# Performance work log

Measured on AMD Instinct MI355X. Metric: run time of the kernel, lower is better.

Reference implementation:

```python
import jax, jax.numpy as jnp
import numpy as np

N_NODES = 50000
N_EDGES = 800000
D_FEAT = 64
K_HOPS = 8


def setup_inputs() -> dict:
    key = jax.random.key(0)
    k1, k2 = jax.random.split(key)
    feature = jax.random.normal(k1, (N_NODES, D_FEAT), dtype=jnp.float32)
    edge_index = jax.random.randint(k2, (2, N_EDGES), 0, N_NODES, dtype=jnp.int32)
    return {"feature": feature, "edge_index": edge_index}


def reference(feature, edge_index):
    # with A_hat = D^{-1/2} (A + I) D^{-1/2} (add_remaining_self_loops + sym_norm).
    n = feature.shape[0]
    src, dst = edge_index[0], edge_index[1]
    # add_remaining_self_loops: drop any existing self-loop edges (weight -> 0)
    # and append a self loop of weight fill_value=1 for every node. Zeroing the
    # weight is mathematically identical to removing the edge.
    ew = jnp.where(src == dst, 0.0, 1.0).astype(feature.dtype)
    loop = jnp.arange(n, dtype=src.dtype)
    row = jnp.concatenate([src, loop])          # message source (x_j)
    col = jnp.concatenate([dst, loop])          # aggregation target (i)
    w = jnp.concatenate([ew, jnp.ones((n,), dtype=feature.dtype)])
    # symmetric normalization: deg over row, norm = d^-1/2[row] * w * d^-1/2[col]
    deg = jax.ops.segment_sum(w, row, num_segments=n)
    deg_inv_sqrt = jnp.where(deg > 0, jax.lax.rsqrt(deg), 0.0)
    norm = deg_inv_sqrt[row] * w * deg_inv_sqrt[col]  # [E+N]

    xs = [feature]
    x = feature
    for _ in range(K_HOPS):  # small fixed K, structural loop
        # gather-scale-scatter_add: out[i] = sum_{(j,i) in E} norm * x[j]
        x = jax.ops.segment_sum(norm[:, None] * x[row], col, num_segments=n)
        xs.append(x)
    return jnp.concatenate(xs, axis=1)  # [N, (K+1)*D]
```

## Files before the change

### kernel.cpp

```cpp
#include <hip/hip_runtime.h>
#include <hip/hip_fp16.h>

#define N_NODES 50000
#define N_EDGES 800000
#define D_FEAT 64
#define K_HOPS 8
#define OUT_STRIDE ((K_HOPS + 1) * D_FEAT)
#define NXCD 8
#define NPART 64
#define PART_CHUNK (N_EDGES / NPART)
#define NWORD (N_NODES / 2)

#define ALIGN256(x) (((x) + 255) & ~(size_t)255)
static const size_t OFF_HISTS = 0;
static const size_t OFF_AUX   = ALIGN256(OFF_HISTS + (size_t)NXCD * N_NODES * 4);
static const size_t AUX_END   = OFF_AUX + (size_t)N_EDGES * 4;
static const size_t XA_BYTES  = (size_t)(N_NODES + 1) * D_FEAT * 2;
static const size_t OFF_XA    = 0;
static const size_t OFF_DINV  = ALIGN256(AUX_END > XA_BYTES ? AUX_END : XA_BYTES);
static const size_t OFF_OFF   = ALIGN256(OFF_DINV  + (size_t)N_NODES * 4);
static const size_t OFF_BSUM  = ALIGN256(OFF_OFF   + (size_t)(N_NODES + 1) * 4);
static const size_t OFF_BASES = ALIGN256(OFF_BSUM  + 64 * 4);
static const size_t OFF_CSR   = ALIGN256(OFF_BASES + (size_t)NXCD * N_NODES * 4);
static const size_t OFF_XB    = ALIGN256(OFF_CSR   + (size_t)N_EDGES * 4);
static const size_t OFF_PART  = OFF_XB;

#define SCAN_BLOCK_ELEMS 1024
#define SCAN_NB ((N_NODES + SCAN_BLOCK_ELEMS - 1) / SCAN_BLOCK_ELEMS)

__device__ __forceinline__ unsigned xcc_id() {
    return __builtin_amdgcn_s_getreg((31u << 11) | 20u) & (NXCD - 1);
}

__device__ __forceinline__ unsigned pack_h2(float a, float b) {
    union { __half2 h; unsigned u; } c;
    c.h = __floats2half2_rn(a, b);
    return c.u;
}
__device__ __forceinline__ float2 unpack_h2(unsigned u) {
    union { unsigned u; __half2 h; } c;
    c.u = u;
    return __half22float2(c.h);
}


__global__ void k_count(const int* __restrict__ src, const int* __restrict__ dst,
                        int* __restrict__ hists, int* __restrict__ aux) {
    int e = blockIdx.x * blockDim.x + threadIdx.x;
    if (e >= N_EDGES) return;
    int s = src[e], d = dst[e];
    if (s == d) { aux[e] = -1; return; }
    unsigned x = xcc_id();
    int pw = __hip_atomic_fetch_add(&hists[x * N_NODES + d], 1,
                                    __ATOMIC_RELAXED, __HIP_MEMORY_SCOPE_WORKGROUP);
    aux[e] = (int)((x << 28) | (unsigned)pw);
}

__global__ __launch_bounds__(256, 1) void k_srcdeg(const int* __restrict__ src,
                                                   const int* __restrict__ dst,
                                                   unsigned* __restrict__ part) {
    __shared__ unsigned h[NWORD];
    int t = threadIdx.x;
    for (int w = t; w < NWORD; w += 256) h[w] = 0u;
    __syncthreads();
    int base = blockIdx.x * PART_CHUNK;
    for (int j = t; j < PART_CHUNK; j += 256) {
        int e = base + j;
        int s = src[e], d = dst[e];
        if (s != d) atomicAdd(&h[s >> 1], (s & 1) ? 65536u : 1u);
    }
    __syncthreads();
    unsigned* out = part + (size_t)blockIdx.x * NWORD;
    for (int w = t; w < NWORD; w += 256) out[w] = h[w];
}

__global__ void k_deg(const unsigned* __restrict__ part, float* __restrict__ dinv) {
    int w = blockIdx.x * blockDim.x + threadIdx.x;
    if (w >= NWORD) return;
    unsigned s0 = 0, s1 = 0, s2 = 0, s3 = 0;
    #pragma unroll 4
    for (int b = 0; b < NPART; b += 4) {
        s0 += part[(size_t)(b + 0) * NWORD + w];
        s1 += part[(size_t)(b + 1) * NWORD + w];
        s2 += part[(size_t)(b + 2) * NWORD + w];
        s3 += part[(size_t)(b + 3) * NWORD + w];
    }
    unsigned s = (s0 + s1) + (s2 + s3);
    dinv[2 * w + 0] = rsqrtf((float)((s & 0xffffu) + 1u));
    dinv[2 * w + 1] = rsqrtf((float)((s >> 16) + 1u));
}

__global__ void k_scan_sums(const int* __restrict__ hists, int* __restrict__ bsum) {
    __shared__ int lds[256];
    int b = blockIdx.x, t = threadIdx.x;
    int base = b * SCAN_BLOCK_ELEMS;
    int s = 0;
    for (int j = t; j < SCAN_BLOCK_ELEMS; j += 256) {
        int idx = base + j;
        if (idx < N_NODES) {
            #pragma unroll
            for (int c = 0; c < NXCD; ++c) s += hists[c * N_NODES + idx];
        }
    }
    lds[t] = s; __syncthreads();
    for (int str = 128; str > 0; str >>= 1) {
        if (t < str) lds[t] += lds[t + str];
        __syncthreads();
    }
    if (t == 0) bsum[b] = lds[0];
}

__global__ void k_scan_top(int* __restrict__ bsum) {
    int lane = threadIdx.x;
    int orig = (lane < SCAN_NB) ? bsum[lane] : 0;
    int v = orig;
    for (int d = 1; d < 64; d <<= 1) {
        int u = __shfl_up(v, d, 64);
        if (lane >= d) v += u;
    }
    if (lane < SCAN_NB) bsum[lane] = v - orig;
}

__global__ void k_scan_down(const int* __restrict__ hists, const int* __restrict__ bsum,
                            int* __restrict__ off, int* __restrict__ bases) {
    __shared__ int lds[256];
    int b = blockIdx.x, t = threadIdx.x;
    int base = b * SCAN_BLOCK_ELEMS + t * 4;
    int tot[4];
    #pragma unroll
    for (int j = 0; j < 4; ++j) {
        int idx = base + j; int s = 0;
        if (idx < N_NODES) {
            #pragma unroll
            for (int c = 0; c < NXCD; ++c) s += hists[c * N_NODES + idx];
        }
        tot[j] = s;
    }
    int tsum = tot[0] + tot[1] + tot[2] + tot[3];
    lds[t] = tsum; __syncthreads();
    int x = tsum;
    for (int d = 1; d < 256; d <<= 1) {
        int u = (t >= d) ? lds[t - d] : 0;
        __syncthreads();
        x += u;
        lds[t] = x;
        __syncthreads();
    }
    int p = (x - tsum) + bsum[b];
    #pragma unroll
    for (int j = 0; j < 4; ++j) {
        int idx = base + j;
        if (idx < N_NODES) {
            off[idx] = p;
            #pragma unroll
            for (int c = 0; c < NXCD; ++c) {
                bases[c * N_NODES + idx] = p;
                p += hists[c * N_NODES + idx];
            }
        } else if (idx == N_NODES) {
            off[idx] = p;
        }
    }
}

__global__ void k_scatter(const int* __restrict__ src, const int* __restrict__ dst,
                          const int* __restrict__ aux, const int* __restrict__ bases,
                          int* __restrict__ csr) {
    int e = blockIdx.x * blockDim.x + threadIdx.x;
    if (e >= N_EDGES) return;
    int a = aux[e];
    if (a < 0) return;
    int s = src[e], d = dst[e];
    unsigned x = (unsigned)a >> 28;
    int pw = a & 0x0FFFFFFF;
    int pos = bases[x * N_NODES + d] + pw;
    csr[pos] = s;
}


__global__ void k_x0(const float4* __restrict__ feat4, float4* __restrict__ out4,
                     uint2* __restrict__ y0, const float* __restrict__ dinv) {
    int t = blockIdx.x * blockDim.x + threadIdx.x;
    if (t >= (N_NODES + 1) * 16) return;
    int row = t >> 4;
    if (row < N_NODES) {
        float4 v = feat4[t];
        out4[(size_t)row * (OUT_STRIDE / 4) + (t & 15)] = v;
        float di = dinv[row];
        uint2 w;
        w.x = pack_h2(v.x * di, v.y * di);
        w.y = pack_h2(v.z * di, v.w * di);
        y0[t] = w;
    } else {
        y0[t] = make_uint2(0u, 0u);
    }
}

template <bool WRITE_HALF>
__global__ __launch_bounds__(256) void k_hop4(
    const uint2* __restrict__ yin,
    float4* __restrict__ outcol4,
    uint2* __restrict__ yout,
    const int* __restrict__ off, const int* __restrict__ csr,
    const float* __restrict__ dinv) {
    int qw = (blockIdx.x * blockDim.x + threadIdx.x) >> 6;
    int lane = threadIdx.x & 63;
    int f = lane & 15;
    int node = qw * 4 + (lane >> 4);
    int e0 = off[node], e1 = off[node + 1];
    float di = dinv[node];
    uint2 sv = yin[node * 16 + f];
    float2 lo = unpack_h2(sv.x), hi = unpack_h2(sv.y);
    float a0 = lo.x, a1 = lo.y, a2 = hi.x, a3 = hi.y;

    int nm = e1 - e0;
    #pragma unroll
    for (int d = 32; d; d >>= 1) nm = max(nm, __shfl_xor(nm, d, 64));

    auto FETCH = [&](int j) -> int {
        int idx = e0 + j;
        int c = csr[idx < e1 ? idx : 0];
        return (idx < e1) ? c : N_NODES;
    };

    int c0 = FETCH(0), c1 = FETCH(1), c2 = FETCH(2), c3 = FETCH(3);
    int c4 = FETCH(4), c5 = FETCH(5), c6 = FETCH(6), c7 = FETCH(7);
    for (int j = 0; j < nm; j += 8) {
        int d0 = FETCH(j + 8),  d1 = FETCH(j + 9),  d2 = FETCH(j + 10), d3 = FETCH(j + 11);
        int d4 = FETCH(j + 12), d5 = FETCH(j + 13), d6 = FETCH(j + 14), d7 = FETCH(j + 15);
        uint2 q0 = yin[c0 * 16 + f];
        uint2 q1 = yin[c1 * 16 + f];
        uint2 q2 = yin[c2 * 16 + f];
        uint2 q3 = yin[c3 * 16 + f];
        uint2 q4 = yin[c4 * 16 + f];
        uint2 q5 = yin[c5 * 16 + f];
        uint2 q6 = yin[c6 * 16 + f];
        uint2 q7 = yin[c7 * 16 + f];
        float2 t;
        t = unpack_h2(q0.x); a0 += t.x; a1 += t.y;
        t = unpack_h2(q0.y); a2 += t.x; a3 += t.y;
        t = unpack_h2(q1.x); a0 += t.x; a1 += t.y;
        t = unpack_h2(q1.y); a2 += t.x; a3 += t.y;
        t = unpack_h2(q2.x); a0 += t.x; a1 += t.y;
        t = unpack_h2(q2.y); a2 += t.x; a3 += t.y;
        t = unpack_h2(q3.x); a0 += t.x; a1 += t.y;
        t = unpack_h2(q3.y); a2 += t.x; a3 += t.y;
        t = unpack_h2(q4.x); a0 += t.x; a1 += t.y;
        t = unpack_h2(q4.y); a2 += t.x; a3 += t.y;
        t = unpack_h2(q5.x); a0 += t.x; a1 += t.y;
        t = unpack_h2(q5.y); a2 += t.x; a3 += t.y;
        t = unpack_h2(q6.x); a0 += t.x; a1 += t.y;
        t = unpack_h2(q6.y); a2 += t.x; a3 += t.y;
        t = unpack_h2(q7.x); a0 += t.x; a1 += t.y;
        t = unpack_h2(q7.y); a2 += t.x; a3 += t.y;
        c0 = d0; c1 = d1; c2 = d2; c3 = d3;
        c4 = d4; c5 = d5; c6 = d6; c7 = d7;
    }

    outcol4[(size_t)node * (OUT_STRIDE / 4) + f] =
        make_float4(di * a0, di * a1, di * a2, di * a3);
    if (WRITE_HALF) {
        float di2 = di * di;
        uint2 w;
        w.x = pack_h2(di2 * a0, di2 * a1);
        w.y = pack_h2(di2 * a2, di2 * a3);
        yout[node * 16 + f] = w;
        if (blockIdx.x == 0 && threadIdx.x < 16)
            yout[N_NODES * 16 + threadIdx.x] = make_uint2(0u, 0u);
    }
}


extern "C" void kernel_launch(void* const* d_in, const int* in_sizes, int n_in,
                              void* d_out, int out_size, void* d_ws, size_t ws_size,
                              hipStream_t stream) {
    const float* feature = (const float*)d_in[0];
    const int* edge = (const int*)d_in[1];
    const int* src = edge;
    const int* dst = edge + N_EDGES;
    float* out = (float*)d_out;
    char* ws = (char*)d_ws;

    int*      hists = (int*)(ws + OFF_HISTS);
    int*      aux   = (int*)(ws + OFF_AUX);
    unsigned* part  = (unsigned*)(ws + OFF_PART);
    float*    dinv  = (float*)(ws + OFF_DINV);
    int*      off   = (int*)(ws + OFF_OFF);
    int*      bsum  = (int*)(ws + OFF_BSUM);
    int*      bases = (int*)(ws + OFF_BASES);
    int*      csr   = (int*)(ws + OFF_CSR);
    uint2*    xa    = (uint2*)(ws + OFF_XA);
    uint2*    xb    = (uint2*)(ws + OFF_XB);

    const int TB = 256;
    hipMemsetAsync(ws + OFF_HISTS, 0, (size_t)NXCD * N_NODES * 4, stream);
    k_count<<<(N_EDGES + TB - 1) / TB, TB, 0, stream>>>(src, dst, hists, aux);
    k_srcdeg<<<NPART, 256, 0, stream>>>(src, dst, part);
    k_deg<<<(NWORD + TB - 1) / TB, TB, 0, stream>>>(part, dinv);
    k_x0<<<((N_NODES + 1) * 16 + TB - 1) / TB, TB, 0, stream>>>(
        (const float4*)feature, (float4*)out, xb, dinv);
    k_scan_sums<<<SCAN_NB, 256, 0, stream>>>(hists, bsum);
    k_scan_top<<<1, 64, 0, stream>>>(bsum);
    k_scan_down<<<SCAN_NB, 256, 0, stream>>>(hists, bsum, off, bases);
    k_scatter<<<(N_EDGES + TB - 1) / TB, TB, 0, stream>>>(src, dst, aux, bases, csr);
    const int hop_blocks = (N_NODES / 4) * 64 / TB;
    for (int k = 1; k <= K_HOPS; ++k) {
        const uint2* yin = (k & 1) ? xb : xa;
        uint2* yout      = (k & 1) ? xa : xb;
        float4* outcol4 = (float4*)out + (size_t)k * 16;
        if (k < K_HOPS)
            k_hop4<true><<<hop_blocks, TB, 0, stream>>>(yin, outcol4, yout, off, csr, dinv);
        else
            k_hop4<false><<<hop_blocks, TB, 0, stream>>>(yin, outcol4, nullptr, off, csr, dinv);
    }
}
```

Measured before the change: 344.1 us.

## Build CSR with per-block LDS histograms instead of global atomics

Replaces the global-atomic, XCD-partitioned destination counting and aux buffer with 128 per-block LDS histograms (packed 16-bit counts) for both source and destination degrees. The scan then derives per-block bases from those partials, and the scatter recomputes local offsets with LDS atomics. The aim is to remove contended global atomics and the memset. The cost is much larger partial arrays: k_scan_down loops over 128 partitions per node and writes 128×N bases, and the scatter only has 128 blocks. The hop kernel's gather unroll is also cut from 8 to 4.

New measurement: 400.9 us. 1.17x slower.

```diff
diff --git a/kernel.cpp b/kernel.cpp
--- a/kernel.cpp
+++ b/kernel.cpp
@@ -6,31 +6,23 @@
 #define D_FEAT 64
 #define K_HOPS 8
 #define OUT_STRIDE ((K_HOPS + 1) * D_FEAT)
-#define NXCD 8
-#define NPART 64
-#define PART_CHUNK (N_EDGES / NPART)
+#define NPART 128
+#define CHUNK (N_EDGES / NPART)
 #define NWORD (N_NODES / 2)
 
+#define SCAN_WORDS 512
+#define SCAN_NB ((NWORD + SCAN_WORDS - 1) / SCAN_WORDS)
+
 #define ALIGN256(x) (((x) + 255) & ~(size_t)255)
-static const size_t OFF_HISTS = 0;
-static const size_t OFF_AUX   = ALIGN256(OFF_HISTS + (size_t)NXCD * N_NODES * 4);
-static const size_t AUX_END   = OFF_AUX + (size_t)N_EDGES * 4;
-static const size_t XA_BYTES  = (size_t)(N_NODES + 1) * D_FEAT * 2;
-static const size_t OFF_XA    = 0;
-static const size_t OFF_DINV  = ALIGN256(AUX_END > XA_BYTES ? AUX_END : XA_BYTES);
-static const size_t OFF_OFF   = ALIGN256(OFF_DINV  + (size_t)N_NODES * 4);
+static const size_t OFF_PSRC  = 0;
+static const size_t OFF_PDST  = OFF_PSRC  + (size_t)NPART * NWORD * 4;
+static const size_t OFF_BASES = OFF_PDST  + (size_t)NPART * NWORD * 4;
+static const size_t OFF_OFF   = ALIGN256(OFF_BASES + (size_t)NPART * N_NODES * 4);
 static const size_t OFF_BSUM  = ALIGN256(OFF_OFF   + (size_t)(N_NODES + 1) * 4);
-static const size_t OFF_BASES = ALIGN256(OFF_BSUM  + 64 * 4);
-static const size_t OFF_CSR   = ALIGN256(OFF_BASES + (size_t)NXCD * N_NODES * 4);
-static const size_t OFF_XB    = ALIGN256(OFF_CSR   + (size_t)N_EDGES * 4);
-static const size_t OFF_PART  = OFF_XB;
-
-#define SCAN_BLOCK_ELEMS 1024
-#define SCAN_NB ((N_NODES + SCAN_BLOCK_ELEMS - 1) / SCAN_BLOCK_ELEMS)
-
-__device__ __forceinline__ unsigned xcc_id() {
-    return __builtin_amdgcn_s_getreg((31u << 11) | 20u) & (NXCD - 1);
-}
+static const size_t OFF_DINV  = ALIGN256(OFF_BSUM  + 64 * 4);
+static const size_t OFF_CSR   = ALIGN256(OFF_DINV  + (size_t)N_NODES * 4);
+static const size_t OFF_XA    = ALIGN256(OFF_CSR   + (size_t)N_EDGES * 4);
+static const size_t OFF_XB    = ALIGN256(OFF_XA + (size_t)(N_NODES + 1) * D_FEAT * 2);
 
 __device__ __forceinline__ unsigned pack_h2(float a, float b) {
     union { __half2 h; unsigned u; } c;
@@ -44,65 +36,61 @@
 }
 
 
-__global__ void k_count(const int* __restrict__ src, const int* __restrict__ dst,
-                        int* __restrict__ hists, int* __restrict__ aux) {
-    int e = blockIdx.x * blockDim.x + threadIdx.x;
-    if (e >= N_EDGES) return;
-    int s = src[e], d = dst[e];
-    if (s == d) { aux[e] = -1; return; }
-    unsigned x = xcc_id();
-    int pw = __hip_atomic_fetch_add(&hists[x * N_NODES + d], 1,
-                                    __ATOMIC_RELAXED, __HIP_MEMORY_SCOPE_WORKGROUP);
-    aux[e] = (int)((x << 28) | (unsigned)pw);
-}
-
-__global__ __launch_bounds__(256, 1) void k_srcdeg(const int* __restrict__ src,
-                                                   const int* __restrict__ dst,
-                                                   unsigned* __restrict__ part) {
+__global__ __launch_bounds__(256, 1) void k_hist(const int* __restrict__ src,
+                                                 const int* __restrict__ dst,
+                                                 unsigned* __restrict__ psrc,
+                                                 unsigned* __restrict__ pdst) {
     __shared__ unsigned h[NWORD];
     int t = threadIdx.x;
+    int base = blockIdx.x * CHUNK;
     for (int w = t; w < NWORD; w += 256) h[w] = 0u;
     __syncthreads();
-    int base = blockIdx.x * PART_CHUNK;
-    for (int j = t; j < PART_CHUNK; j += 256) {
-        int e = base + j;
-        int s = src[e], d = dst[e];
+    for (int j = t; j < CHUNK; j += 256) {
+        int s = src[base + j], d = dst[base + j];
         if (s != d) atomicAdd(&h[s >> 1], (s & 1) ? 65536u : 1u);
     }
     __syncthreads();
-    unsigned* out = part + (size_t)blockIdx.x * NWORD;
-    for (int w = t; w < NWORD; w += 256) out[w] = h[w];
-}
-
-__global__ void k_deg(const unsigned* __restrict__ part, float* __restrict__ dinv) {
+    unsigned* o1 = psrc + (size_t)blockIdx.x * NWORD;
+    for (int w = t; w < NWORD; w += 256) o1[w] = h[w];
+    __syncthreads();
+    for (int w = t; w < NWORD; w += 256) h[w] = 0u;
+    __syncthreads();
+    for (int j = t; j < CHUNK; j += 256) {
+        int s = src[base + j], d = dst[base + j];
+        if (s != d) atomicAdd(&h[d >> 1], (d & 1) ? 65536u : 1u);
+    }
+    __syncthreads();
+    unsigned* o2 = pdst + (size_t)blockIdx.x * NWORD;
+    for (int w = t; w < NWORD; w += 256) o2[w] = h[w];
+}
+
+__global__ void k_deg(const unsigned* __restrict__ psrc, float* __restrict__ dinv) {
     int w = blockIdx.x * blockDim.x + threadIdx.x;
     if (w >= NWORD) return;
     unsigned s0 = 0, s1 = 0, s2 = 0, s3 = 0;
     #pragma unroll 4
-    for (int b = 0; b < NPART; b += 4) {
-        s0 += part[(size_t)(b + 0) * NWORD + w];
-        s1 += part[(size_t)(b + 1) * NWORD + w];
-        s2 += part[(size_t)(b + 2) * NWORD + w];
-        s3 += part[(size_t)(b + 3) * NWORD + w];
+    for (int c = 0; c < NPART; c += 4) {
+        s0 += psrc[(size_t)(c + 0) * NWORD + w];
+        s1 += psrc[(size_t)(c + 1) * NWORD + w];
+        s2 += psrc[(size_t)(c + 2) * NWORD + w];
+        s3 += psrc[(size_t)(c + 3) * NWORD + w];
     }
     unsigned s = (s0 + s1) + (s2 + s3);
     dinv[2 * w + 0] = rsqrtf((float)((s & 0xffffu) + 1u));
     dinv[2 * w + 1] = rsqrtf((float)((s >> 16) + 1u));
 }
 
-__global__ void k_scan_sums(const int* __restrict__ hists, int* __restrict__ bsum) {
+__global__ void k_scan_sums(const unsigned* __restrict__ pdst, int* __restrict__ bsum) {
     __shared__ int lds[256];
     int b = blockIdx.x, t = threadIdx.x;
-    int base = b * SCAN_BLOCK_ELEMS;
-    int s = 0;
-    for (int j = t; j < SCAN_BLOCK_ELEMS; j += 256) {
-        int idx = base + j;
-        if (idx < N_NODES) {
-            #pragma unroll
-            for (int c = 0; c < NXCD; ++c) s += hists[c * N_NODES + idx];
-        }
-    }
-    lds[t] = s; __syncthreads();
+    int wend = min((b + 1) * SCAN_WORDS, NWORD);
+    unsigned tot = 0;
+    for (int w = b * SCAN_WORDS + t; w < wend; w += 256) {
+        unsigned s = 0;
+        for (int c = 0; c < NPART; ++c) s += pdst[(size_t)c * NWORD + w];
+        tot += (s & 0xffffu) + (s >> 16);
+    }
+    lds[t] = (int)tot; __syncthreads();
     for (int str = 128; str > 0; str >>= 1) {
         if (t < str) lds[t] += lds[t + str];
         __syncthreads();
@@ -121,22 +109,20 @@
     if (lane < SCAN_NB) bsum[lane] = v - orig;
 }
 
-__global__ void k_scan_down(const int* __restrict__ hists, const int* __restrict__ bsum,
+__global__ void k_scan_down(const unsigned* __restrict__ pdst, const int* __restrict__ bsum,
                             int* __restrict__ off, int* __restrict__ bases) {
     __shared__ int lds[256];
     int b = blockIdx.x, t = threadIdx.x;
-    int base = b * SCAN_BLOCK_ELEMS + t * 4;
-    int tot[4];
-    #pragma unroll
-    for (int j = 0; j < 4; ++j) {
-        int idx = base + j; int s = 0;
-        if (idx < N_NODES) {
-            #pragma unroll
-            for (int c = 0; c < NXCD; ++c) s += hists[c * N_NODES + idx];
-        }
-        tot[j] = s;
-    }
-    int tsum = tot[0] + tot[1] + tot[2] + tot[3];
+    int w0 = b * SCAN_WORDS + 2 * t;
+    unsigned t0 = 0, t1 = 0;
+    for (int c = 0; c < NPART; ++c) {
+        const unsigned* pc = pdst + (size_t)c * NWORD;
+        if (w0 < NWORD)     t0 += pc[w0];
+        if (w0 + 1 < NWORD) t1 += pc[w0 + 1];
+    }
+    int n[4] = { (int)(t0 & 0xffffu), (int)(t0 >> 16),
+                 (int)(t1 & 0xffffu), (int)(t1 >> 16) };
+    int tsum = (n[0] + n[1]) + (n[2] + n[3]);
     lds[t] = tsum; __syncthreads();
     int x = tsum;
     for (int d = 1; d < 256; d <<= 1) {
@@ -149,32 +135,41 @@
     int p = (x - tsum) + bsum[b];
     #pragma unroll
     for (int j = 0; j < 4; ++j) {
-        int idx = base + j;
-        if (idx < N_NODES) {
-            off[idx] = p;
-            #pragma unroll
-            for (int c = 0; c < NXCD; ++c) {
-                bases[c * N_NODES + idx] = p;
-                p += hists[c * N_NODES + idx];
+        int node = 2 * w0 + j;
+        if (node < N_NODES) {
+            off[node] = p;
+            int w = node >> 1;
+            bool hi = node & 1;
+            int acc = p;
+            for (int c = 0; c < NPART; ++c) {
+                bases[(size_t)c * N_NODES + node] = acc;
+                unsigned v = pdst[(size_t)c * NWORD + w];
+                acc += hi ? (int)(v >> 16) : (int)(v & 0xffffu);
             }
-        } else if (idx == N_NODES) {
-            off[idx] = p;
+            p = acc;
+        } else if (node == N_NODES) {
+            off[node] = p;
         }
     }
 }
 
-__global__ void k_scatter(const int* __restrict__ src, const int* __restrict__ dst,
-                          const int* __restrict__ aux, const int* __restrict__ bases,
-                          int* __restrict__ csr) {
-    int e = blockIdx.x * blockDim.x + threadIdx.x;
-    if (e >= N_EDGES) return;
-    int a = aux[e];
-    if (a < 0) return;
-    int s = src[e], d = dst[e];
-    unsigned x = (unsigned)a >> 28;
-    int pw = a & 0x0FFFFFFF;
-    int pos = bases[x * N_NODES + d] + pw;
-    csr[pos] = s;
+__global__ __launch_bounds__(256, 1) void k_scatter(const int* __restrict__ src,
+                                                    const int* __restrict__ dst,
+                                                    const int* __restrict__ bases,
+                                                    int* __restrict__ csr) {
+    __shared__ unsigned h[NWORD];
+    int t = threadIdx.x;
+    int base = blockIdx.x * CHUNK;
+    const int* bp = bases + (size_t)blockIdx.x * N_NODES;
+    for (int w = t; w < NWORD; w += 256) h[w] = 0u;
+    __syncthreads();
+    for (int j = t; j < CHUNK; j += 256) {
+        int s = src[base + j], d = dst[base + j];
+        if (s == d) continue;
+        unsigned old = atomicAdd(&h[d >> 1], (d & 1) ? 65536u : 1u);
+        unsigned pw = (d & 1) ? (old >> 16) : (old & 0xffffu);
+        csr[bp[d] + (int)pw] = s;
+    }
 }
 
 
@@ -224,18 +219,12 @@
     };
 
     int c0 = FETCH(0), c1 = FETCH(1), c2 = FETCH(2), c3 = FETCH(3);
-    int c4 = FETCH(4), c5 = FETCH(5), c6 = FETCH(6), c7 = FETCH(7);
-    for (int j = 0; j < nm; j += 8) {
-        int d0 = FETCH(j + 8),  d1 = FETCH(j + 9),  d2 = FETCH(j + 10), d3 = FETCH(j + 11);
-        int d4 = FETCH(j + 12), d5 = FETCH(j + 13), d6 = FETCH(j + 14), d7 = FETCH(j + 15);
+    for (int j = 0; j < nm; j += 4) {
+        int d0 = FETCH(j + 4), d1 = FETCH(j + 5), d2 = FETCH(j + 6), d3 = FETCH(j + 7);
         uint2 q0 = yin[c0 * 16 + f];
         uint2 q1 = yin[c1 * 16 + f];
         uint2 q2 = yin[c2 * 16 + f];
         uint2 q3 = yin[c3 * 16 + f];
-        uint2 q4 = yin[c4 * 16 + f];
-        uint2 q5 = yin[c5 * 16 + f];
-        uint2 q6 = yin[c6 * 16 + f];
-        uint2 q7 = yin[c7 * 16 + f];
         float2 t;
         t = unpack_h2(q0.x); a0 += t.x; a1 += t.y;
         t = unpack_h2(q0.y); a2 += t.x; a3 += t.y;
@@ -245,16 +234,7 @@
         t = unpack_h2(q2.y); a2 += t.x; a3 += t.y;
         t = unpack_h2(q3.x); a0 += t.x; a1 += t.y;
         t = unpack_h2(q3.y); a2 += t.x; a3 += t.y;
-        t = unpack_h2(q4.x); a0 += t.x; a1 += t.y;
-        t = unpack_h2(q4.y); a2 += t.x; a3 += t.y;
-        t = unpack_h2(q5.x); a0 += t.x; a1 += t.y;
-        t = unpack_h2(q5.y); a2 += t.x; a3 += t.y;
-        t = unpack_h2(q6.x); a0 += t.x; a1 += t.y;
-        t = unpack_h2(q6.y); a2 += t.x; a3 += t.y;
-        t = unpack_h2(q7.x); a0 += t.x; a1 += t.y;
-        t = unpack_h2(q7.y); a2 += t.x; a3 += t.y;
         c0 = d0; c1 = d1; c2 = d2; c3 = d3;
-        c4 = d4; c5 = d5; c6 = d6; c7 = d7;
     }
 
     outcol4[(size_t)node * (OUT_STRIDE / 4) + f] =
@@ -281,28 +261,25 @@
     float* out = (float*)d_out;
     char* ws = (char*)d_ws;
 
-    int*      hists = (int*)(ws + OFF_HISTS);
-    int*      aux   = (int*)(ws + OFF_AUX);
-    unsigned* part  = (unsigned*)(ws + OFF_PART);
-    float*    dinv  = (float*)(ws + OFF_DINV);
+    unsigned* psrc  = (unsigned*)(ws + OFF_PSRC);
+    unsigned* pdst  = (unsigned*)(ws + OFF_PDST);
+    int*      bases = (int*)(ws + OFF_BASES);
     int*      off   = (int*)(ws + OFF_OFF);
     int*      bsum  = (int*)(ws + OFF_BSUM);
-    int*      bases = (int*)(ws + OFF_BASES);
+    float*    dinv  = (float*)(ws + OFF_DINV);
     int*      csr   = (int*)(ws + OFF_CSR);
     uint2*    xa    = (uint2*)(ws + OFF_XA);
     uint2*    xb    = (uint2*)(ws + OFF_XB);
 
     const int TB = 256;
-    hipMemsetAsync(ws + OFF_HISTS, 0, (size_t)NXCD * N_NODES * 4, stream);
-    k_count<<<(N_EDGES + TB - 1) / TB, TB, 0, stream>>>(src, dst, hists, aux);
-    k_srcdeg<<<NPART, 256, 0, stream>>>(src, dst, part);
-    k_deg<<<(NWORD + TB - 1) / TB, TB, 0, stream>>>(part, dinv);
+    k_hist<<<NPART, 256, 0, stream>>>(src, dst, psrc, pdst);
+    k_deg<<<(NWORD + TB - 1) / TB, TB, 0, stream>>>(psrc, dinv);
     k_x0<<<((N_NODES + 1) * 16 + TB - 1) / TB, TB, 0, stream>>>(
         (const float4*)feature, (float4*)out, xb, dinv);
-    k_scan_sums<<<SCAN_NB, 256, 0, stream>>>(hists, bsum);
+    k_scan_sums<<<SCAN_NB, 256, 0, stream>>>(pdst, bsum);
     k_scan_top<<<1, 64, 0, stream>>>(bsum);
-    k_scan_down<<<SCAN_NB, 256, 0, stream>>>(hists, bsum, off, bases);
-    k_scatter<<<(N_EDGES + TB - 1) / TB, TB, 0, stream>>>(src, dst, aux, bases, csr);
+    k_scan_down<<<SCAN_NB, 256, 0, stream>>>(pdst, bsum, off, bases);
+    k_scatter<<<NPART, 256, 0, stream>>>(src, dst, bases, csr);
     const int hop_blocks = (N_NODES / 4) * 64 / TB;
     for (int k = 1; k <= K_HOPS; ++k) {
         const uint2* yin = (k & 1) ? xb : xa;
```
